# Optimization experiments

Measured on AMD Instinct MI355X. Metric: run time of the kernel, lower is better.

The kernel has to match this reference:

```python
import jax, jax.numpy as jnp
import numpy as np

N = 100000   # nodes
D = 128      # in_feats
H = 128      # hidden_size
E = 500000   # message edges
EP = 100000  # positive pair edges
EN = 500000  # negative pair edges


def setup_inputs() -> dict:
    key = jax.random.key(0)
    ks = jax.random.split(key, 20)
    s = 1.0 / np.sqrt(H)
    f32 = jnp.float32
    inp = {
        "x": jax.random.normal(ks[0], (N, D), f32),
        "src": jax.random.randint(ks[1], (E,), 0, N, jnp.int32),
        "dst": jax.random.randint(ks[2], (E,), 0, N, jnp.int32),
        "pos_src": jax.random.randint(ks[3], (EP,), 0, N, jnp.int32),
        "pos_dst": jax.random.randint(ks[4], (EP,), 0, N, jnp.int32),
        "neg_src": jax.random.randint(ks[5], (EN,), 0, N, jnp.int32),
        "neg_dst": jax.random.randint(ks[6], (EN,), 0, N, jnp.int32),
        # SAGEConv layer 0 (in->hid) and layer 1 (hid->hid)
        "W_self0": jax.random.normal(ks[7], (D, H), f32) * s,
        "W_neigh0": jax.random.normal(ks[8], (D, H), f32) * s,
        "b0": jnp.zeros((H,), f32),
        "W_self1": jax.random.normal(ks[9], (H, H), f32) * s,
        "W_neigh1": jax.random.normal(ks[10], (H, H), f32) * s,
        "b1": jnp.zeros((H,), f32),
        # EdgeDecoder MLP: hid->hid->hid->1
        "dW1": jax.random.normal(ks[11], (H, H), f32) * s,
        "db1": jnp.zeros((H,), f32),
        "dW2": jax.random.normal(ks[12], (H, H), f32) * s,
        "db2": jnp.zeros((H,), f32),
        "dW3": jax.random.normal(ks[13], (H, 1), f32) * s,
        "db3": jnp.zeros((1,), f32),
    }
    return inp


def _sage_mean(h, src, dst, W_self, W_neigh, b, n_nodes):
    # mean-aggregate neighbor features: gather src feats, segment-sum over dst
    agg = jax.ops.segment_sum(h[src], dst, num_segments=n_nodes)       # [N, d]
    deg = jax.ops.segment_sum(jnp.ones((src.shape[0],), h.dtype), dst,
                              num_segments=n_nodes)                     # [N]
    h_neigh = agg / jnp.maximum(deg, 1.0)[:, None]
    return h @ W_self + h_neigh @ W_neigh + b


def _edge_decode(h, e_src, e_dst, W1, b1, W2, b2, W3, b3):
    z = h[e_src] * h[e_dst]                    # [E_pair, H]
    z = jax.nn.relu(z @ W1 + b1)
    z = jax.nn.relu(z @ W2 + b2)
    return z @ W3 + b3                         # [E_pair, 1]


def reference(x, src, dst, pos_src, pos_dst, neg_src, neg_dst,
              W_self0, W_neigh0, b0, W_self1, W_neigh1, b1,
              dW1, db1, dW2, db2, dW3, db3):
    n = x.shape[0]
    h = jax.nn.relu(_sage_mean(x, src, dst, W_self0, W_neigh0, b0, n))
    h = _sage_mean(h, src, dst, W_self1, W_neigh1, b1, n)  # no act on last layer
    h_pos = _edge_decode(h, pos_src, pos_dst, dW1, db1, dW2, db2, dW3, db3)
    h_neg = _edge_decode(h, neg_src, neg_dst, dW1, db1, dW2, db2, dW3, db3)
    return (h_pos, h_neg)
```

## Files before the change

kernel.cpp:

```cpp
#include <hip/hip_runtime.h>
#include <hip/hip_bf16.h>

#define HD 128

typedef unsigned int u32;
typedef unsigned short u16;
typedef __attribute__((ext_vector_type(8))) short short8;
typedef __attribute__((ext_vector_type(4))) float f32x4;

__device__ __forceinline__ float bf2f(u16 u) {
    return __uint_as_float(((u32)u) << 16);
}
__device__ __forceinline__ u16 f2bf(float f) {
    u32 u = __float_as_uint(f);
    u32 r = (u + 0x7fffu + ((u >> 16) & 1u)) >> 16;
    return (u16)r;
}
__device__ __forceinline__ u32 pk2bf(float lo, float hi) {
    __hip_bfloat162 h = __float22bfloat162_rn(make_float2(lo, hi));
    union { __hip_bfloat162 h; u32 u; } cv; cv.h = h;
    return cv.u;
}
__device__ __forceinline__ u32 hmul2(u32 a, u32 b) {
    union { u32 u; __hip_bfloat162 h; } x, y, r;
    x.u = a; y.u = b;
    r.h = __hmul2(x.h, y.h);
    return r.u;
}
__device__ __forceinline__ float ldf(const void* p, size_t i, bool f32m) {
    return f32m ? ((const float*)p)[i] : bf2f(((const u16*)p)[i]);
}
__device__ __forceinline__ int swz(int row, int col) {
    return row * 128 + ((((col >> 3) ^ (row & 7)) << 3) | (col & 7));
}

__global__ void detect_mode(const u32* __restrict__ x, int* __restrict__ mode) {
    __shared__ int cnt_s;
    if (threadIdx.x == 0) cnt_s = 0;
    __syncthreads();
    u32 e = (x[threadIdx.x] >> 23) & 0xFFu;
    if (e >= 90u && e < 170u) atomicAdd(&cnt_s, 1);
    __syncthreads();
    if (threadIdx.x == 0) mode[0] = (cnt_s >= 128) ? 1 : 0;
}

__global__ void pack_w6(const void* __restrict__ W0, const void* __restrict__ W1,
                        const void* __restrict__ W2, const void* __restrict__ W3,
                        const void* __restrict__ W4, const void* __restrict__ W5,
                        u16* __restrict__ out, const int* __restrict__ gmode) {
    const bool f32m = gmode[0] != 0;
    int gid = blockIdx.x * 256 + threadIdx.x;
    if (gid >= 6 * 16384) return;
    int sel = gid >> 14, idx = gid & 16383;
    const void* W = sel == 0 ? W0 : sel == 1 ? W1 : sel == 2 ? W2 :
                    sel == 3 ? W3 : sel == 4 ? W4 : W5;
    int j = idx & 7, lane = (idx >> 3) & 63, ks = (idx >> 9) & 3, nt = idx >> 11;
    int k = ks * 32 + (lane >> 4) * 8 + j;
    int n = nt * 16 + (lane & 15);
    out[gid] = f2bf(ldf(W, (size_t)k * HD + n, f32m));
}

__global__ void cnt_count(const int* __restrict__ dst, int* __restrict__ cnt, int e) {
    int i = blockIdx.x * 256 + threadIdx.x;
    if (i < e) atomicAdd(&cnt[dst[i]], 1);
}

__global__ void scan_blocks(const int* __restrict__ cnt, int* __restrict__ rowptr,
                            int* __restrict__ bsum, int n) {
    __shared__ int s[256];
    int t = threadIdx.x, gid = blockIdx.x * 256 + t;
    int v = (gid < n) ? cnt[gid] : 0;
    s[t] = v; __syncthreads();
    #pragma unroll
    for (int off = 1; off < 256; off <<= 1) {
        int x = (t >= off) ? s[t - off] : 0;
        __syncthreads();
        s[t] += x;
        __syncthreads();
    }
    if (gid < n) rowptr[gid] = s[t] - v;
    if (t == 255) bsum[blockIdx.x] = s[255];
}

__global__ void scan_bsum(int* __restrict__ bsum, int nb) {
    __shared__ int s[1024];
    __shared__ int carry;
    int t = threadIdx.x;
    if (t == 0) carry = 0;
    __syncthreads();
    for (int base = 0; base < nb; base += 1024) {
        int i = base + t;
        int v = (i < nb) ? bsum[i] : 0;
        s[t] = v; __syncthreads();
        #pragma unroll
        for (int off = 1; off < 1024; off <<= 1) {
            int x = (t >= off) ? s[t - off] : 0;
            __syncthreads();
            s[t] += x;
            __syncthreads();
        }
        if (i < nb) bsum[i] = carry + s[t] - v;
        __syncthreads();
        if (t == 0) carry += s[1023];
        __syncthreads();
    }
}

__global__ void scan_add(int* __restrict__ rowptr, const int* __restrict__ bsum,
                         int n, int e) {
    int gid = blockIdx.x * 256 + threadIdx.x;
    if (gid < n) rowptr[gid] += bsum[blockIdx.x];
    else if (gid == n) rowptr[n] = e;
}

__global__ void csr_fill(const int* __restrict__ src, const int* __restrict__ dst,
                         const int* __restrict__ rowptr, int* __restrict__ cur,
                         int* __restrict__ cidx, int e) {
    int i = blockIdx.x * 256 + threadIdx.x;
    if (i >= e) return;
    int d = dst[i];
    int p = rowptr[d] + atomicAdd(&cur[d], 1);
    cidx[p] = src[i];
}

__global__ __launch_bounds__(256) void agg_gather(
    const void* __restrict__ h, const int* __restrict__ rowptr,
    const int* __restrict__ cidx, u16* __restrict__ aggb,
    const int* __restrict__ gmode, int use_mode, int n) {
    const bool f32m = use_mode && (gmode[0] != 0);
    int wid = (blockIdx.x * 256 + threadIdx.x) >> 6;
    int lane = threadIdx.x & 63;
    if (wid >= n) return;
    int l16 = lane & 15, g = lane >> 4;
    int s0 = rowptr[wid], s1 = rowptr[wid + 1];
    float acc[8] = {0.f, 0.f, 0.f, 0.f, 0.f, 0.f, 0.f, 0.f};
    for (int i = s0 + g; i < s1; i += 4) {
        int s = cidx[i];
        if (f32m) {
            const float* p = (const float*)h + (size_t)s * HD + l16 * 8;
            float4 a = *(const float4*)p, b = *(const float4*)(p + 4);
            acc[0] += a.x; acc[1] += a.y; acc[2] += a.z; acc[3] += a.w;
            acc[4] += b.x; acc[5] += b.y; acc[6] += b.z; acc[7] += b.w;
        } else {
            uint4 v = *(const uint4*)((const u16*)h + (size_t)s * HD + l16 * 8);
            acc[0] += __uint_as_float(v.x << 16); acc[1] += __uint_as_float(v.x & 0xffff0000u);
            acc[2] += __uint_as_float(v.y << 16); acc[3] += __uint_as_float(v.y & 0xffff0000u);
            acc[4] += __uint_as_float(v.z << 16); acc[5] += __uint_as_float(v.z & 0xffff0000u);
            acc[6] += __uint_as_float(v.w << 16); acc[7] += __uint_as_float(v.w & 0xffff0000u);
        }
    }
    #pragma unroll
    for (int k = 0; k < 8; k++) {
        acc[k] += __shfl_xor(acc[k], 16);
        acc[k] += __shfl_xor(acc[k], 32);
    }
    if (g == 0) {
        float iv = 1.f / fmaxf((float)(s1 - s0), 1.f);
        uint4 o;
        o.x = pk2bf(acc[0] * iv, acc[1] * iv);
        o.y = pk2bf(acc[2] * iv, acc[3] * iv);
        o.z = pk2bf(acc[4] * iv, acc[5] * iv);
        o.w = pk2bf(acc[6] * iv, acc[7] * iv);
        *(uint4*)&aggb[(size_t)wid * HD + l16 * 8] = o;
    }
}

template <bool RELU>
__global__ __launch_bounds__(256) void sage_mfma(
    const void* __restrict__ X, const u16* __restrict__ aggb,
    const u16* __restrict__ Wsp, const u16* __restrict__ Wnp,
    const void* __restrict__ bias, u16* __restrict__ hout,
    const int* __restrict__ gmode, int use_mode, int n) {
    __shared__ u16 zS[64 * 128];
    __shared__ u16 zN[64 * 128];
    u16* outh = zS;

    const bool f32m = gmode[0] != 0;
    const bool inf32 = use_mode && f32m;
    const int t = threadIdx.x;
    const int n0 = blockIdx.x * 64;
    const int lane = t & 63;
    const int w = t >> 6;
    const int cl = lane & 15, quad = lane >> 4;

    #pragma unroll
    for (int i = 0; i < 4; i++) {
        int idx = t + i * 256;
        int e = idx >> 4, sg = (idx & 15) * 8;
        int node = n0 + e;
        uint4 p = make_uint4(0, 0, 0, 0), q = make_uint4(0, 0, 0, 0);
        if (node < n) {
            if (inf32) {
                const float* xp = (const float*)X + (size_t)node * HD + sg;
                float4 v0 = *(const float4*)xp, v1 = *(const float4*)(xp + 4);
                p.x = pk2bf(v0.x, v0.y); p.y = pk2bf(v0.z, v0.w);
                p.z = pk2bf(v1.x, v1.y); p.w = pk2bf(v1.z, v1.w);
            } else {
                p = *(const uint4*)((const u16*)X + (size_t)node * HD + sg);
            }
            q = *(const uint4*)&aggb[(size_t)node * HD + sg];
        }
        int sa = swz(e, sg);
        *(uint4*)&zS[sa] = p;
        *(uint4*)&zN[sa] = q;
    }
    __syncthreads();

    f32x4 acc[2][4];
    #pragma unroll
    for (int ft = 0; ft < 2; ft++) {
        int f0 = w * 32 + ft * 16 + quad * 4;
        f32x4 bv;
        bv[0] = ldf(bias, f0 + 0, f32m);
        bv[1] = ldf(bias, f0 + 1, f32m);
        bv[2] = ldf(bias, f0 + 2, f32m);
        bv[3] = ldf(bias, f0 + 3, f32m);
        #pragma unroll
        for (int et = 0; et < 4; et++) acc[ft][et] = bv;
    }
    #pragma unroll
    for (int ks = 0; ks < 4; ks++) {
        short8 aS[2], aN[2], bS[4], bN[4];
        #pragma unroll
        for (int ft = 0; ft < 2; ft++) {
            aS[ft] = ((const short8*)Wsp)[((w * 2 + ft) * 4 + ks) * 64 + lane];
            aN[ft] = ((const short8*)Wnp)[((w * 2 + ft) * 4 + ks) * 64 + lane];
        }
        #pragma unroll
        for (int et = 0; et < 4; et++) {
            int sa = swz(et * 16 + cl, ks * 32 + quad * 8);
            bS[et] = *(const short8*)&zS[sa];
            bN[et] = *(const short8*)&zN[sa];
        }
        #pragma unroll
        for (int ft = 0; ft < 2; ft++)
            #pragma unroll
            for (int et = 0; et < 4; et++) {
                acc[ft][et] = __builtin_amdgcn_mfma_f32_16x16x32_bf16(
                    aS[ft], bS[et], acc[ft][et], 0, 0, 0);
                acc[ft][et] = __builtin_amdgcn_mfma_f32_16x16x32_bf16(
                    aN[ft], bN[et], acc[ft][et], 0, 0, 0);
            }
    }
    __syncthreads();

    #pragma unroll
    for (int ft = 0; ft < 2; ft++) {
        int f0 = w * 32 + ft * 16 + quad * 4;
        #pragma unroll
        for (int et = 0; et < 4; et++) {
            f32x4 v = acc[ft][et];
            float v0 = RELU ? fmaxf(v[0], 0.f) : v[0];
            float v1 = RELU ? fmaxf(v[1], 0.f) : v[1];
            float v2 = RELU ? fmaxf(v[2], 0.f) : v[2];
            float v3 = RELU ? fmaxf(v[3], 0.f) : v[3];
            *(uint2*)&outh[swz(et * 16 + cl, f0)] =
                make_uint2(pk2bf(v0, v1), pk2bf(v2, v3));
        }
    }
    __syncthreads();
    #pragma unroll
    for (int i = 0; i < 4; i++) {
        int idx = t + i * 256;
        int e = idx >> 4, sg = (idx & 15) * 8;
        int node = n0 + e;
        if (node < n)
            *(uint4*)&hout[(size_t)node * HD + sg] = *(const uint4*)&outh[swz(e, sg)];
    }
}

__device__ __forceinline__ void gemm128(
    const u16* zin, u16* zout, const u16* __restrict__ Wp,
    const void* __restrict__ bias, bool f32m, int w, int lane) {
    const int cl = lane & 15, quad = lane >> 4;
    f32x4 acc[2][4];
    #pragma unroll
    for (int ft = 0; ft < 2; ft++) {
        int f0 = w * 32 + ft * 16 + quad * 4;
        f32x4 bv;
        bv[0] = ldf(bias, f0 + 0, f32m);
        bv[1] = ldf(bias, f0 + 1, f32m);
        bv[2] = ldf(bias, f0 + 2, f32m);
        bv[3] = ldf(bias, f0 + 3, f32m);
        #pragma unroll
        for (int et = 0; et < 4; et++) acc[ft][et] = bv;
    }
    #pragma unroll
    for (int ks = 0; ks < 4; ks++) {
        short8 a[2], b[4];
        #pragma unroll
        for (int ft = 0; ft < 2; ft++)
            a[ft] = ((const short8*)Wp)[((w * 2 + ft) * 4 + ks) * 64 + lane];
        #pragma unroll
        for (int et = 0; et < 4; et++)
            b[et] = *(const short8*)&zin[swz(et * 16 + cl, ks * 32 + quad * 8)];
        #pragma unroll
        for (int ft = 0; ft < 2; ft++)
            #pragma unroll
            for (int et = 0; et < 4; et++)
                acc[ft][et] = __builtin_amdgcn_mfma_f32_16x16x32_bf16(
                    a[ft], b[et], acc[ft][et], 0, 0, 0);
    }
    #pragma unroll
    for (int ft = 0; ft < 2; ft++) {
        int f0 = w * 32 + ft * 16 + quad * 4;
        #pragma unroll
        for (int et = 0; et < 4; et++) {
            f32x4 v = acc[ft][et];
            *(uint2*)&zout[swz(et * 16 + cl, f0)] = make_uint2(
                pk2bf(fmaxf(v[0], 0.f), fmaxf(v[1], 0.f)),
                pk2bf(fmaxf(v[2], 0.f), fmaxf(v[3], 0.f)));
        }
    }
}

__global__ __launch_bounds__(256) void edge_decode_mfma(
    const u16* __restrict__ h,
    const int* __restrict__ psrc, const int* __restrict__ pdst, int ep, int PB,
    const int* __restrict__ nsrc, const int* __restrict__ ndst, int en,
    const u16* __restrict__ W1p, const void* __restrict__ b1,
    const u16* __restrict__ W2p, const void* __restrict__ b2,
    const void* __restrict__ W3, const void* __restrict__ b3,
    void* __restrict__ out, const int* __restrict__ gmode) {
    __shared__ u16 zA[64 * 128];
    __shared__ u16 zB[64 * 128];
    __shared__ float psum[256];
    const bool f32m = gmode[0] != 0;
    const int t = threadIdx.x;
    const int b = blockIdx.x;
    const int* esrc; const int* edst; int e0, obase, ne;
    if (b < PB) { esrc = psrc; edst = pdst; e0 = b * 64;        obase = 0;  ne = ep; }
    else        { esrc = nsrc; edst = ndst; e0 = (b - PB) * 64; obase = ep; ne = en; }
    const int lane = t & 63;
    const int w = t >> 6;
    const int cl = lane & 15, quad = lane >> 4;

    #pragma unroll
    for (int i = 0; i < 4; i++) {
        int idx = t + i * 256;
        int e = idx >> 4, sg = (idx & 15) * 8;
        int eg = e0 + e;
        uint4 z = make_uint4(0, 0, 0, 0);
        if (eg < ne) {
            int s = esrc[eg], d = edst[eg];
            uint4 a  = *(const uint4*)(h + (size_t)s * HD + sg);
            uint4 bv = *(const uint4*)(h + (size_t)d * HD + sg);
            z.x = hmul2(a.x, bv.x); z.y = hmul2(a.y, bv.y);
            z.z = hmul2(a.z, bv.z); z.w = hmul2(a.w, bv.w);
        }
        *(uint4*)&zA[swz(e, sg)] = z;
    }
    __syncthreads();

    gemm128(zA, zB, W1p, b1, f32m, w, lane);
    __syncthreads();

    f32x4 acc[2][4];
    #pragma unroll
    for (int ft = 0; ft < 2; ft++) {
        int f0 = w * 32 + ft * 16 + quad * 4;
        f32x4 bv;
        bv[0] = ldf(b2, f0 + 0, f32m);
        bv[1] = ldf(b2, f0 + 1, f32m);
        bv[2] = ldf(b2, f0 + 2, f32m);
        bv[3] = ldf(b2, f0 + 3, f32m);
        #pragma unroll
        for (int et = 0; et < 4; et++) acc[ft][et] = bv;
    }
    #pragma unroll
    for (int ks = 0; ks < 4; ks++) {
        short8 a[2], bb[4];
        #pragma unroll
        for (int ft = 0; ft < 2; ft++)
            a[ft] = ((const short8*)W2p)[((w * 2 + ft) * 4 + ks) * 64 + lane];
        #pragma unroll
        for (int et = 0; et < 4; et++)
            bb[et] = *(const short8*)&zB[swz(et * 16 + cl, ks * 32 + quad * 8)];
        #pragma unroll
        for (int ft = 0; ft < 2; ft++)
            #pragma unroll
            for (int et = 0; et < 4; et++)
                acc[ft][et] = __builtin_amdgcn_mfma_f32_16x16x32_bf16(
                    a[ft], bb[et], acc[ft][et], 0, 0, 0);
    }
    float p[4] = {0.f, 0.f, 0.f, 0.f};
    #pragma unroll
    for (int ft = 0; ft < 2; ft++) {
        int f0 = w * 32 + ft * 16 + quad * 4;
        float w3v0 = ldf(W3, f0 + 0, f32m);
        float w3v1 = ldf(W3, f0 + 1, f32m);
        float w3v2 = ldf(W3, f0 + 2, f32m);
        float w3v3 = ldf(W3, f0 + 3, f32m);
        #pragma unroll
        for (int et = 0; et < 4; et++) {
            f32x4 v = acc[ft][et];
            p[et] = fmaf(fmaxf(v[0], 0.f), w3v0, p[et]);
            p[et] = fmaf(fmaxf(v[1], 0.f), w3v1, p[et]);
            p[et] = fmaf(fmaxf(v[2], 0.f), w3v2, p[et]);
            p[et] = fmaf(fmaxf(v[3], 0.f), w3v3, p[et]);
        }
    }
    #pragma unroll
    for (int et = 0; et < 4; et++) {
        p[et] += __shfl_xor(p[et], 16);
        p[et] += __shfl_xor(p[et], 32);
    }
    if (lane < 16) {
        #pragma unroll
        for (int et = 0; et < 4; et++)
            psum[w * 64 + et * 16 + lane] = p[et];
    }
    __syncthreads();
    if (t < 64) {
        int eg = e0 + t;
        if (eg < ne) {
            float sum = ldf(b3, 0, f32m) + (psum[t] + psum[64 + t])
                      + (psum[128 + t] + psum[192 + t]);
            if (f32m) ((float*)out)[obase + eg] = sum;
            else      ((u16*)out)[obase + eg]   = f2bf(sum);
        }
    }
}

extern "C" void kernel_launch(void* const* d_in, const int* in_sizes, int n_in,
                              void* d_out, int out_size, void* d_ws, size_t ws_size,
                              hipStream_t stream) {
    const void* x      = d_in[0];
    const int* src     = (const int*)d_in[1];
    const int* dst     = (const int*)d_in[2];
    const int* pos_src = (const int*)d_in[3];
    const int* pos_dst = (const int*)d_in[4];
    const int* neg_src = (const int*)d_in[5];
    const int* neg_dst = (const int*)d_in[6];
    const void* Ws0 = d_in[7];
    const void* Wn0 = d_in[8];
    const void* b0  = d_in[9];
    const void* Ws1 = d_in[10];
    const void* Wn1 = d_in[11];
    const void* b1  = d_in[12];
    const void* dW1 = d_in[13];
    const void* db1 = d_in[14];
    const void* dW2 = d_in[15];
    const void* db2 = d_in[16];
    const void* dW3 = d_in[17];
    const void* db3 = d_in[18];

    const int n  = in_sizes[0] / HD;
    const int e  = in_sizes[1];
    const int ep = in_sizes[3];
    const int en = in_sizes[5];
    const int NB = (n + 255) / 256;
    const int PB = (ep + 63) / 64, NDB = (en + 63) / 64;

    char* base = (char*)d_ws;
    u16* aggb = (u16*)d_ws;
    u16* h1   = aggb + (size_t)n * HD;
    size_t off = (size_t)n * HD * 4;
    int* mode = (int*)(base + off);      off += 16;
    int* rowptr = (int*)(base + off);    off += (size_t)(n + 1) * 4; off = (off + 15) & ~(size_t)15;
    int* cnt = (int*)(base + off);       off += (size_t)n * 4;       off = (off + 15) & ~(size_t)15;
    int* cidx = (int*)(base + off);      off += (size_t)e * 4;       off = (off + 15) & ~(size_t)15;
    int* bsum = (int*)(base + off);      off += (size_t)NB * 4;      off = (off + 15) & ~(size_t)15;
    u16* Wpk  = (u16*)(base + off);
    u16* W1p  = Wpk;
    u16* W2p  = Wpk + 16384;
    u16* Ws0p = Wpk + 2 * 16384;
    u16* Wn0p = Wpk + 3 * 16384;
    u16* Ws1p = Wpk + 4 * 16384;
    u16* Wn1p = Wpk + 5 * 16384;

    detect_mode<<<dim3(1), dim3(256), 0, stream>>>((const u32*)x, mode);

    hipMemsetAsync(cnt, 0, (size_t)n * 4, stream);
    cnt_count<<<dim3((e + 255) / 256), dim3(256), 0, stream>>>(dst, cnt, e);
    scan_blocks<<<dim3(NB), dim3(256), 0, stream>>>(cnt, rowptr, bsum, n);
    scan_bsum<<<dim3(1), dim3(1024), 0, stream>>>(bsum, NB);
    scan_add<<<dim3((n + 256) / 256), dim3(256), 0, stream>>>(rowptr, bsum, n, e);
    hipMemsetAsync(cnt, 0, (size_t)n * 4, stream);
    csr_fill<<<dim3((e + 255) / 256), dim3(256), 0, stream>>>(src, dst, rowptr, cnt, cidx, e);

    pack_w6<<<dim3(384), dim3(256), 0, stream>>>(dW1, dW2, Ws0, Wn0, Ws1, Wn1, Wpk, mode);

    agg_gather<<<dim3((n * 64 + 255) / 256), dim3(256), 0, stream>>>(
        x, rowptr, cidx, aggb, mode, 1, n);
    sage_mfma<true><<<dim3((n + 63) / 64), dim3(256), 0, stream>>>(
        x, aggb, Ws0p, Wn0p, b0, h1, mode, 1, n);

    agg_gather<<<dim3((n * 64 + 255) / 256), dim3(256), 0, stream>>>(
        h1, rowptr, cidx, aggb, mode, 0, n);
    sage_mfma<false><<<dim3((n + 63) / 64), dim3(256), 0, stream>>>(
        h1, aggb, Ws1p, Wn1p, b1, aggb , mode, 0, n);

    edge_decode_mfma<<<dim3(PB + NDB), dim3(256), 0, stream>>>(
        aggb, pos_src, pos_dst, ep, PB, neg_src, neg_dst, en,
        W1p, db1, W2p, db2, dW3, db3, d_out, mode);
}
```

Measured before the change: 377.4 us.

## Persistent MFMA kernels with register-resident weights and single-pass CSR fill

The SAGE and edge-decoder MFMA kernels become persistent grid-stride loops over 64-row tiles on a capped grid. Each block loads its weight fragments and biases into registers once instead of per tile. The CSR fill now atomically bumps a cursor array that scan_add initialises from rowptr, which drops one memset and one rowptr load per edge. The risks are higher register pressure from holding the weight fragments, which may lower occupancy, and less latency hiding because tile loads are no longer overlapped across many blocks.

```diff
diff --git a/kernel.cpp b/kernel.cpp
--- a/kernel.cpp
+++ b/kernel.cpp
@@ -107,19 +107,22 @@
 }
 
 __global__ void scan_add(int* __restrict__ rowptr, const int* __restrict__ bsum,
-                         int n, int e) {
+                         int* __restrict__ cur, int n, int e) {
     int gid = blockIdx.x * 256 + threadIdx.x;
-    if (gid < n) rowptr[gid] += bsum[blockIdx.x];
-    else if (gid == n) rowptr[n] = e;
+    if (gid < n) {
+        int v = rowptr[gid] + bsum[blockIdx.x];
+        rowptr[gid] = v;
+        cur[gid] = v;
+    } else if (gid == n) {
+        rowptr[n] = e;
+    }
 }
 
 __global__ void csr_fill(const int* __restrict__ src, const int* __restrict__ dst,
-                         const int* __restrict__ rowptr, int* __restrict__ cur,
-                         int* __restrict__ cidx, int e) {
+                         int* __restrict__ cur, int* __restrict__ cidx, int e) {
     int i = blockIdx.x * 256 + threadIdx.x;
     if (i >= e) return;
-    int d = dst[i];
-    int p = rowptr[d] + atomicAdd(&cur[d], 1);
+    int p = atomicAdd(&cur[dst[i]], 1);
     cidx[p] = src[i];
 }
 
@@ -170,7 +173,7 @@
     const void* __restrict__ X, const u16* __restrict__ aggb,
     const u16* __restrict__ Wsp, const u16* __restrict__ Wnp,
     const void* __restrict__ bias, u16* __restrict__ hout,
-    const int* __restrict__ gmode, int use_mode, int n) {
+    const int* __restrict__ gmode, int use_mode, int n, int ntiles) {
     __shared__ u16 zS[64 * 128];
     __shared__ u16 zN[64 * 128];
     u16* outh = zS;
@@ -178,146 +181,109 @@
     const bool f32m = gmode[0] != 0;
     const bool inf32 = use_mode && f32m;
     const int t = threadIdx.x;
-    const int n0 = blockIdx.x * 64;
     const int lane = t & 63;
     const int w = t >> 6;
     const int cl = lane & 15, quad = lane >> 4;
 
-    #pragma unroll
-    for (int i = 0; i < 4; i++) {
-        int idx = t + i * 256;
-        int e = idx >> 4, sg = (idx & 15) * 8;
-        int node = n0 + e;
-        uint4 p = make_uint4(0, 0, 0, 0), q = make_uint4(0, 0, 0, 0);
-        if (node < n) {
-            if (inf32) {
-                const float* xp = (const float*)X + (size_t)node * HD + sg;
-                float4 v0 = *(const float4*)xp, v1 = *(const float4*)(xp + 4);
-                p.x = pk2bf(v0.x, v0.y); p.y = pk2bf(v0.z, v0.w);
-                p.z = pk2bf(v1.x, v1.y); p.w = pk2bf(v1.z, v1.w);
-            } else {
-                p = *(const uint4*)((const u16*)X + (size_t)node * HD + sg);
-            }
-            q = *(const uint4*)&aggb[(size_t)node * HD + sg];
-        }
-        int sa = swz(e, sg);
-        *(uint4*)&zS[sa] = p;
-        *(uint4*)&zN[sa] = q;
-    }
-    __syncthreads();
-
-    f32x4 acc[2][4];
+    short8 aS[2][4], aN[2][4];
+    f32x4 bv[2];
     #pragma unroll
     for (int ft = 0; ft < 2; ft++) {
+        #pragma unroll
+        for (int ks = 0; ks < 4; ks++) {
+            aS[ft][ks] = ((const short8*)Wsp)[((w * 2 + ft) * 4 + ks) * 64 + lane];
+            aN[ft][ks] = ((const short8*)Wnp)[((w * 2 + ft) * 4 + ks) * 64 + lane];
+        }
         int f0 = w * 32 + ft * 16 + quad * 4;
-        f32x4 bv;
-        bv[0] = ldf(bias, f0 + 0, f32m);
-        bv[1] = ldf(bias, f0 + 1, f32m);
-        bv[2] = ldf(bias, f0 + 2, f32m);
-        bv[3] = ldf(bias, f0 + 3, f32m);
-        #pragma unroll
-        for (int et = 0; et < 4; et++) acc[ft][et] = bv;
-    }
-    #pragma unroll
-    for (int ks = 0; ks < 4; ks++) {
-        short8 aS[2], aN[2], bS[4], bN[4];
+        bv[ft][0] = ldf(bias, f0 + 0, f32m);
+        bv[ft][1] = ldf(bias, f0 + 1, f32m);
+        bv[ft][2] = ldf(bias, f0 + 2, f32m);
+        bv[ft][3] = ldf(bias, f0 + 3, f32m);
+    }
+
+    for (int tile = blockIdx.x; tile < ntiles; tile += gridDim.x) {
+        const int n0 = tile * 64;
+
+        #pragma unroll
+        for (int i = 0; i < 4; i++) {
+            int idx = t + i * 256;
+            int e = idx >> 4, sg = (idx & 15) * 8;
+            int node = n0 + e;
+            uint4 p = make_uint4(0, 0, 0, 0), q = make_uint4(0, 0, 0, 0);
+            if (node < n) {
+                if (inf32) {
+                    const float* xp = (const float*)X + (size_t)node * HD + sg;
+                    float4 v0 = *(const float4*)xp, v1 = *(const float4*)(xp + 4);
+                    p.x = pk2bf(v0.x, v0.y); p.y = pk2bf(v0.z, v0.w);
+                    p.z = pk2bf(v1.x, v1.y); p.w = pk2bf(v1.z, v1.w);
+                } else {
+                    p = *(const uint4*)((const u16*)X + (size_t)node * HD + sg);
+                }
+                q = *(const uint4*)&aggb[(size_t)node * HD + sg];
+            }
+            int sa = swz(e, sg);
+            *(uint4*)&zS[sa] = p;
+            *(uint4*)&zN[sa] = q;
+        }
+        __syncthreads();
+
+        f32x4 acc[2][4];
+        #pragma unroll
+        for (int ft = 0; ft < 2; ft++)
+            #pragma unroll
+            for (int et = 0; et < 4; et++) acc[ft][et] = bv[ft];
+        #pragma unroll
+        for (int ks = 0; ks < 4; ks++) {
+            short8 bS[4], bN[4];
+            #pragma unroll
+            for (int et = 0; et < 4; et++) {
+                int sa = swz(et * 16 + cl, ks * 32 + quad * 8);
+                bS[et] = *(const short8*)&zS[sa];
+                bN[et] = *(const short8*)&zN[sa];
+            }
+            #pragma unroll
+            for (int ft = 0; ft < 2; ft++)
+                #pragma unroll
+                for (int et = 0; et < 4; et++) {
+                    acc[ft][et] = __builtin_amdgcn_mfma_f32_16x16x32_bf16(
+                        aS[ft][ks], bS[et], acc[ft][et], 0, 0, 0);
+                    acc[ft][et] = __builtin_amdgcn_mfma_f32_16x16x32_bf16(
+                        aN[ft][ks], bN[et], acc[ft][et], 0, 0, 0);
+                }
+        }
+        __syncthreads();
+
         #pragma unroll
         for (int ft = 0; ft < 2; ft++) {
-            aS[ft] = ((const short8*)Wsp)[((w * 2 + ft) * 4 + ks) * 64 + lane];
-            aN[ft] = ((const short8*)Wnp)[((w * 2 + ft) * 4 + ks) * 64 + lane];
-        }
-        #pragma unroll
-        for (int et = 0; et < 4; et++) {
-            int sa = swz(et * 16 + cl, ks * 32 + quad * 8);
-            bS[et] = *(const short8*)&zS[sa];
-            bN[et] = *(const short8*)&zN[sa];
-        }
-        #pragma unroll
-        for (int ft = 0; ft < 2; ft++)
+            int f0 = w * 32 + ft * 16 + quad * 4;
             #pragma unroll
             for (int et = 0; et < 4; et++) {
-                acc[ft][et] = __builtin_amdgcn_mfma_f32_16x16x32_bf16(
-                    aS[ft], bS[et], acc[ft][et], 0, 0, 0);
-                acc[ft][et] = __builtin_amdgcn_mfma_f32_16x16x32_bf16(
-                    aN[ft], bN[et], acc[ft][et], 0, 0, 0);
-            }
-    }
-    __syncthreads();
-
-    #pragma unroll
-    for (int ft = 0; ft < 2; ft++) {
-        int f0 = w * 32 + ft * 16 + quad * 4;
-        #pragma unroll
-        for (int et = 0; et < 4; et++) {
-            f32x4 v = acc[ft][et];
-            float v0 = RELU ? fmaxf(v[0], 0.f) : v[0];
-            float v1 = RELU ? fmaxf(v[1], 0.f) : v[1];
-            float v2 = RELU ? fmaxf(v[2], 0.f) : v[2];
-            float v3 = RELU ? fmaxf(v[3], 0.f) : v[3];
-            *(uint2*)&outh[swz(et * 16 + cl, f0)] =
-                make_uint2(pk2bf(v0, v1), pk2bf(v2, v3));
-        }
-    }
-    __syncthreads();
-    #pragma unroll
-    for (int i = 0; i < 4; i++) {
-        int idx = t + i * 256;
-        int e = idx >> 4, sg = (idx & 15) * 8;
-        int node = n0 + e;
-        if (node < n)
-            *(uint4*)&hout[(size_t)node * HD + sg] = *(const uint4*)&outh[swz(e, sg)];
-    }
-}
-
-__device__ __forceinline__ void gemm128(
-    const u16* zin, u16* zout, const u16* __restrict__ Wp,
-    const void* __restrict__ bias, bool f32m, int w, int lane) {
-    const int cl = lane & 15, quad = lane >> 4;
-    f32x4 acc[2][4];
-    #pragma unroll
-    for (int ft = 0; ft < 2; ft++) {
-        int f0 = w * 32 + ft * 16 + quad * 4;
-        f32x4 bv;
-        bv[0] = ldf(bias, f0 + 0, f32m);
-        bv[1] = ldf(bias, f0 + 1, f32m);
-        bv[2] = ldf(bias, f0 + 2, f32m);
-        bv[3] = ldf(bias, f0 + 3, f32m);
-        #pragma unroll
-        for (int et = 0; et < 4; et++) acc[ft][et] = bv;
-    }
-    #pragma unroll
-    for (int ks = 0; ks < 4; ks++) {
-        short8 a[2], b[4];
-        #pragma unroll
-        for (int ft = 0; ft < 2; ft++)
-            a[ft] = ((const short8*)Wp)[((w * 2 + ft) * 4 + ks) * 64 + lane];
-        #pragma unroll
-        for (int et = 0; et < 4; et++)
-            b[et] = *(const short8*)&zin[swz(et * 16 + cl, ks * 32 + quad * 8)];
-        #pragma unroll
-        for (int ft = 0; ft < 2; ft++)
-            #pragma unroll
-            for (int et = 0; et < 4; et++)
-                acc[ft][et] = __builtin_amdgcn_mfma_f32_16x16x32_bf16(
-                    a[ft], b[et], acc[ft][et], 0, 0, 0);
-    }
-    #pragma unroll
-    for (int ft = 0; ft < 2; ft++) {
-        int f0 = w * 32 + ft * 16 + quad * 4;
-        #pragma unroll
-        for (int et = 0; et < 4; et++) {
-            f32x4 v = acc[ft][et];
-            *(uint2*)&zout[swz(et * 16 + cl, f0)] = make_uint2(
-                pk2bf(fmaxf(v[0], 0.f), fmaxf(v[1], 0.f)),
-                pk2bf(fmaxf(v[2], 0.f), fmaxf(v[3], 0.f)));
-        }
+                f32x4 v = acc[ft][et];
+                float v0 = RELU ? fmaxf(v[0], 0.f) : v[0];
+                float v1 = RELU ? fmaxf(v[1], 0.f) : v[1];
+                float v2 = RELU ? fmaxf(v[2], 0.f) : v[2];
+                float v3 = RELU ? fmaxf(v[3], 0.f) : v[3];
+                *(uint2*)&outh[swz(et * 16 + cl, f0)] =
+                    make_uint2(pk2bf(v0, v1), pk2bf(v2, v3));
+            }
+        }
+        __syncthreads();
+        #pragma unroll
+        for (int i = 0; i < 4; i++) {
+            int idx = t + i * 256;
+            int e = idx >> 4, sg = (idx & 15) * 8;
+            int node = n0 + e;
+            if (node < n)
+                *(uint4*)&hout[(size_t)node * HD + sg] = *(const uint4*)&outh[swz(e, sg)];
+        }
+        __syncthreads();
     }
 }
 
 __global__ __launch_bounds__(256) void edge_decode_mfma(
     const u16* __restrict__ h,
     const int* __restrict__ psrc, const int* __restrict__ pdst, int ep, int PB,
-    const int* __restrict__ nsrc, const int* __restrict__ ndst, int en,
+    const int* __restrict__ nsrc, const int* __restrict__ ndst, int en, int TB,
     const u16* __restrict__ W1p, const void* __restrict__ b1,
     const u16* __restrict__ W2p, const void* __restrict__ b2,
     const void* __restrict__ W3, const void* __restrict__ b3,
@@ -327,98 +293,133 @@
     __shared__ float psum[256];
     const bool f32m = gmode[0] != 0;
     const int t = threadIdx.x;
-    const int b = blockIdx.x;
-    const int* esrc; const int* edst; int e0, obase, ne;
-    if (b < PB) { esrc = psrc; edst = pdst; e0 = b * 64;        obase = 0;  ne = ep; }
-    else        { esrc = nsrc; edst = ndst; e0 = (b - PB) * 64; obase = ep; ne = en; }
     const int lane = t & 63;
     const int w = t >> 6;
     const int cl = lane & 15, quad = lane >> 4;
 
-    #pragma unroll
-    for (int i = 0; i < 4; i++) {
-        int idx = t + i * 256;
-        int e = idx >> 4, sg = (idx & 15) * 8;
-        int eg = e0 + e;
-        uint4 z = make_uint4(0, 0, 0, 0);
-        if (eg < ne) {
-            int s = esrc[eg], d = edst[eg];
-            uint4 a  = *(const uint4*)(h + (size_t)s * HD + sg);
-            uint4 bv = *(const uint4*)(h + (size_t)d * HD + sg);
-            z.x = hmul2(a.x, bv.x); z.y = hmul2(a.y, bv.y);
-            z.z = hmul2(a.z, bv.z); z.w = hmul2(a.w, bv.w);
-        }
-        *(uint4*)&zA[swz(e, sg)] = z;
-    }
-    __syncthreads();
-
-    gemm128(zA, zB, W1p, b1, f32m, w, lane);
-    __syncthreads();
-
-    f32x4 acc[2][4];
+    short8 w1f[2][4], w2f[2][4];
+    f32x4 bv1[2], bv2[2], w3v[2];
     #pragma unroll
     for (int ft = 0; ft < 2; ft++) {
+        #pragma unroll
+        for (int ks = 0; ks < 4; ks++) {
+            w1f[ft][ks] = ((const short8*)W1p)[((w * 2 + ft) * 4 + ks) * 64 + lane];
+            w2f[ft][ks] = ((const short8*)W2p)[((w * 2 + ft) * 4 + ks) * 64 + lane];
+        }
         int f0 = w * 32 + ft * 16 + quad * 4;
-        f32x4 bv;
-        bv[0] = ldf(b2, f0 + 0, f32m);
-        bv[1] = ldf(b2, f0 + 1, f32m);
-        bv[2] = ldf(b2, f0 + 2, f32m);
-        bv[3] = ldf(b2, f0 + 3, f32m);
-        #pragma unroll
-        for (int et = 0; et < 4; et++) acc[ft][et] = bv;
-    }
-    #pragma unroll
-    for (int ks = 0; ks < 4; ks++) {
-        short8 a[2], bb[4];
+        #pragma unroll
+        for (int r = 0; r < 4; r++) {
+            bv1[ft][r] = ldf(b1, f0 + r, f32m);
+            bv2[ft][r] = ldf(b2, f0 + r, f32m);
+            w3v[ft][r] = ldf(W3, f0 + r, f32m);
+        }
+    }
+    const float b3v = ldf(b3, 0, f32m);
+
+    for (int tile = blockIdx.x; tile < TB; tile += gridDim.x) {
+        const int* esrc; const int* edst; int e0, obase, ne;
+        if (tile < PB) { esrc = psrc; edst = pdst; e0 = tile * 64;        obase = 0;  ne = ep; }
+        else           { esrc = nsrc; edst = ndst; e0 = (tile - PB) * 64; obase = ep; ne = en; }
+
+        #pragma unroll
+        for (int i = 0; i < 4; i++) {
+            int idx = t + i * 256;
+            int e = idx >> 4, sg = (idx & 15) * 8;
+            int eg = e0 + e;
+            uint4 z = make_uint4(0, 0, 0, 0);
+            if (eg < ne) {
+                int s = esrc[eg], d = edst[eg];
+                uint4 a  = *(const uint4*)(h + (size_t)s * HD + sg);
+                uint4 bb = *(const uint4*)(h + (size_t)d * HD + sg);
+                z.x = hmul2(a.x, bb.x); z.y = hmul2(a.y, bb.y);
+                z.z = hmul2(a.z, bb.z); z.w = hmul2(a.w, bb.w);
+            }
+            *(uint4*)&zA[swz(e, sg)] = z;
+        }
+        __syncthreads();
+
+        {
+            f32x4 acc[2][4];
+            #pragma unroll
+            for (int ft = 0; ft < 2; ft++)
+                #pragma unroll
+                for (int et = 0; et < 4; et++) acc[ft][et] = bv1[ft];
+            #pragma unroll
+            for (int ks = 0; ks < 4; ks++) {
+                short8 b[4];
+                #pragma unroll
+                for (int et = 0; et < 4; et++)
+                    b[et] = *(const short8*)&zA[swz(et * 16 + cl, ks * 32 + quad * 8)];
+                #pragma unroll
+                for (int ft = 0; ft < 2; ft++)
+                    #pragma unroll
+                    for (int et = 0; et < 4; et++)
+                        acc[ft][et] = __builtin_amdgcn_mfma_f32_16x16x32_bf16(
+                            w1f[ft][ks], b[et], acc[ft][et], 0, 0, 0);
+            }
+            #pragma unroll
+            for (int ft = 0; ft < 2; ft++) {
+                int f0 = w * 32 + ft * 16 + quad * 4;
+                #pragma unroll
+                for (int et = 0; et < 4; et++) {
+                    f32x4 v = acc[ft][et];
+                    *(uint2*)&zB[swz(et * 16 + cl, f0)] = make_uint2(
+                        pk2bf(fmaxf(v[0], 0.f), fmaxf(v[1], 0.f)),
+                        pk2bf(fmaxf(v[2], 0.f), fmaxf(v[3], 0.f)));
+                }
+            }
+        }
+        __syncthreads();
+
+        f32x4 acc[2][4];
         #pragma unroll
         for (int ft = 0; ft < 2; ft++)
-            a[ft] = ((const short8*)W2p)[((w * 2 + ft) * 4 + ks) * 64 + lane];
-        #pragma unroll
-        for (int et = 0; et < 4; et++)
-            bb[et] = *(const short8*)&zB[swz(et * 16 + cl, ks * 32 + quad * 8)];
+            #pragma unroll
+            for (int et = 0; et < 4; et++) acc[ft][et] = bv2[ft];
+        #pragma unroll
+        for (int ks = 0; ks < 4; ks++) {
+            short8 bb[4];
+            #pragma unroll
+            for (int et = 0; et < 4; et++)
+                bb[et] = *(const short8*)&zB[swz(et * 16 + cl, ks * 32 + quad * 8)];
+            #pragma unroll
+            for (int ft = 0; ft < 2; ft++)
+                #pragma unroll
+                for (int et = 0; et < 4; et++)
+                    acc[ft][et] = __builtin_amdgcn_mfma_f32_16x16x32_bf16(
+                        w2f[ft][ks], bb[et], acc[ft][et], 0, 0, 0);
+        }
+        float p[4] = {0.f, 0.f, 0.f, 0.f};
         #pragma unroll
         for (int ft = 0; ft < 2; ft++)
             #pragma unroll
+            for (int et = 0; et < 4; et++) {
+                f32x4 v = acc[ft][et];
+                p[et] = fmaf(fmaxf(v[0], 0.f), w3v[ft][0], p[et]);
+                p[et] = fmaf(fmaxf(v[1], 0.f), w3v[ft][1], p[et]);
+                p[et] = fmaf(fmaxf(v[2], 0.f), w3v[ft][2], p[et]);
+                p[et] = fmaf(fmaxf(v[3], 0.f), w3v[ft][3], p[et]);
+            }
+        #pragma unroll
+        for (int et = 0; et < 4; et++) {
+            p[et] += __shfl_xor(p[et], 16);
+            p[et] += __shfl_xor(p[et], 32);
+        }
+        if (lane < 16) {
+            #pragma unroll
             for (int et = 0; et < 4; et++)
-                acc[ft][et] = __builtin_amdgcn_mfma_f32_16x16x32_bf16(
-                    a[ft], bb[et], acc[ft][et], 0, 0, 0);
-    }
-    float p[4] = {0.f, 0.f, 0.f, 0.f};
-    #pragma unroll
-    for (int ft = 0; ft < 2; ft++) {
-        int f0 = w * 32 + ft * 16 + quad * 4;
-        float w3v0 = ldf(W3, f0 + 0, f32m);
-        float w3v1 = ldf(W3, f0 + 1, f32m);
-        float w3v2 = ldf(W3, f0 + 2, f32m);
-        float w3v3 = ldf(W3, f0 + 3, f32m);
-        #pragma unroll
-        for (int et = 0; et < 4; et++) {
-            f32x4 v = acc[ft][et];
-            p[et] = fmaf(fmaxf(v[0], 0.f), w3v0, p[et]);
-            p[et] = fmaf(fmaxf(v[1], 0.f), w3v1, p[et]);
-            p[et] = fmaf(fmaxf(v[2], 0.f), w3v2, p[et]);
-            p[et] = fmaf(fmaxf(v[3], 0.f), w3v3, p[et]);
-        }
-    }
-    #pragma unroll
-    for (int et = 0; et < 4; et++) {
-        p[et] += __shfl_xor(p[et], 16);
-        p[et] += __shfl_xor(p[et], 32);
-    }
-    if (lane < 16) {
-        #pragma unroll
-        for (int et = 0; et < 4; et++)
-            psum[w * 64 + et * 16 + lane] = p[et];
-    }
-    __syncthreads();
-    if (t < 64) {
-        int eg = e0 + t;
-        if (eg < ne) {
-            float sum = ldf(b3, 0, f32m) + (psum[t] + psum[64 + t])
-                      + (psum[128 + t] + psum[192 + t]);
-            if (f32m) ((float*)out)[obase + eg] = sum;
-            else      ((u16*)out)[obase + eg]   = f2bf(sum);
-        }
+                psum[w * 64 + et * 16 + lane] = p[et];
+        }
+        __syncthreads();
+        if (t < 64) {
+            int eg = e0 + t;
+            if (eg < ne) {
+                float sum = b3v + (psum[t] + psum[64 + t]) + (psum[128 + t] + psum[192 + t]);
+                if (f32m) ((float*)out)[obase + eg] = sum;
+                else      ((u16*)out)[obase + eg]   = f2bf(sum);
+            }
+        }
+        __syncthreads();
     }
 }
 
@@ -451,6 +452,7 @@
     const int en = in_sizes[5];
     const int NB = (n + 255) / 256;
     const int PB = (ep + 63) / 64, NDB = (en + 63) / 64;
+    const int NT = (n + 63) / 64;
 
     char* base = (char*)d_ws;
     u16* aggb = (u16*)d_ws;
@@ -458,7 +460,7 @@
     size_t off = (size_t)n * HD * 4;
     int* mode = (int*)(base + off);      off += 16;
     int* rowptr = (int*)(base + off);    off += (size_t)(n + 1) * 4; off = (off + 15) & ~(size_t)15;
-    int* cnt = (int*)(base + off);       off += (size_t)n * 4;       off = (off + 15) & ~(size_t)15;
+    int* cur = (int*)(base + off);       off += (size_t)n * 4;       off = (off + 15) & ~(size_t)15;
     int* cidx = (int*)(base + off);      off += (size_t)e * 4;       off = (off + 15) & ~(size_t)15;
     int* bsum = (int*)(base + off);      off += (size_t)NB * 4;      off = (off + 15) & ~(size_t)15;
     u16* Wpk  = (u16*)(base + off);
@@ -471,27 +473,28 @@
 
     detect_mode<<<dim3(1), dim3(256), 0, stream>>>((const u32*)x, mode);
 
-    hipMemsetAsync(cnt, 0, (size_t)n * 4, stream);
-    cnt_count<<<dim3((e + 255) / 256), dim3(256), 0, stream>>>(dst, cnt, e);
-    scan_blocks<<<dim3(NB), dim3(256), 0, stream>>>(cnt, rowptr, bsum, n);
+    hipMemsetAsync(cur, 0, (size_t)n * 4, stream);
+    cnt_count<<<dim3((e + 255) / 256), dim3(256), 0, stream>>>(dst, cur, e);
+    scan_blocks<<<dim3(NB), dim3(256), 0, stream>>>(cur, rowptr, bsum, n);
     scan_bsum<<<dim3(1), dim3(1024), 0, stream>>>(bsum, NB);
-    scan_add<<<dim3((n + 256) / 256), dim3(256), 0, stream>>>(rowptr, bsum, n, e);
-    hipMemsetAsync(cnt, 0, (size_t)n * 4, stream);
-    csr_fill<<<dim3((e + 255) / 256), dim3(256), 0, stream>>>(src, dst, rowptr, cnt, cidx, e);
+    scan_add<<<dim3((n + 256) / 256), dim3(256), 0, stream>>>(rowptr, bsum, cur, n, e);
+    csr_fill<<<dim3((e + 255) / 256), dim3(256), 0, stream>>>(src, dst, cur, cidx, e);
 
     pack_w6<<<dim3(384), dim3(256), 0, stream>>>(dW1, dW2, Ws0, Wn0, Ws1, Wn1, Wpk, mode);
 
     agg_gather<<<dim3((n * 64 + 255) / 256), dim3(256), 0, stream>>>(
         x, rowptr, cidx, aggb, mode, 1, n);
-    sage_mfma<true><<<dim3((n + 63) / 64), dim3(256), 0, stream>>>(
-        x, aggb, Ws0p, Wn0p, b0, h1, mode, 1, n);
+    sage_mfma<true><<<dim3(1024), dim3(256), 0, stream>>>(
+        x, aggb, Ws0p, Wn0p, b0, h1, mode, 1, n, NT);
 
     agg_gather<<<dim3((n * 64 + 255) / 256), dim3(256), 0, stream>>>(
         h1, rowptr, cidx, aggb, mode, 0, n);
-    sage_mfma<false><<<dim3((n + 63) / 64), dim3(256), 0, stream>>>(
-        h1, aggb, Ws1p, Wn1p, b1, aggb , mode, 0, n);
-
-    edge_decode_mfma<<<dim3(PB + NDB), dim3(256), 0, stream>>>(
-        aggb, pos_src, pos_dst, ep, PB, neg_src, neg_dst, en,
+    sage_mfma<false><<<dim3(1024), dim3(256), 0, stream>>>(
+        h1, aggb, Ws1p, Wn1p, b1, aggb , mode, 0, n, NT);
+
+    int TB = PB + NDB;
+    int db = TB < 1024 ? TB : 1024;
+    edge_decode_mfma<<<dim3(db), dim3(256), 0, stream>>>(
+        aggb, pos_src, pos_dst, ep, PB, neg_src, neg_dst, en, TB,
         W1p, db1, W2p, db2, dW3, db3, d_out, mode);
 }
```

Result: slower. 398.6 us (+5.6%).

## Halve shared memory in sage and decode kernels; seed CSR cursor in scan

Applied to the files above, without the earlier changes.

The SAGE GEMM kernel now stages self and neighbor inputs through one shared buffer in two sequential phases instead of two buffers at once. The edge decoder reuses a single tile for both MLP layers in place, and the gemm128 helper is inlined. Both kernels drop from 32 KB to about 16 KB of LDS per block, which should allow more resident blocks per CU. Separately, scan_add writes the row offsets into the cursor array, removing a memset and a rowptr load from csr_fill. The cost is extra barriers and serialized staging of the neighbor tile in the SAGE kernel.

```diff
diff --git a/kernel.cpp b/kernel.cpp
--- a/kernel.cpp
+++ b/kernel.cpp
@@ -107,19 +107,22 @@
 }
 
 __global__ void scan_add(int* __restrict__ rowptr, const int* __restrict__ bsum,
-                         int n, int e) {
+                         int* __restrict__ cur, int n, int e) {
     int gid = blockIdx.x * 256 + threadIdx.x;
-    if (gid < n) rowptr[gid] += bsum[blockIdx.x];
-    else if (gid == n) rowptr[n] = e;
+    if (gid < n) {
+        int v = rowptr[gid] + bsum[blockIdx.x];
+        rowptr[gid] = v;
+        cur[gid] = v;
+    } else if (gid == n) {
+        rowptr[n] = e;
+    }
 }
 
 __global__ void csr_fill(const int* __restrict__ src, const int* __restrict__ dst,
-                         const int* __restrict__ rowptr, int* __restrict__ cur,
-                         int* __restrict__ cidx, int e) {
+                         int* __restrict__ cur, int* __restrict__ cidx, int e) {
     int i = blockIdx.x * 256 + threadIdx.x;
     if (i >= e) return;
-    int d = dst[i];
-    int p = rowptr[d] + atomicAdd(&cur[d], 1);
+    int p = atomicAdd(&cur[dst[i]], 1);
     cidx[p] = src[i];
 }
 
@@ -171,10 +174,7 @@
     const u16* __restrict__ Wsp, const u16* __restrict__ Wnp,
     const void* __restrict__ bias, u16* __restrict__ hout,
     const int* __restrict__ gmode, int use_mode, int n) {
-    __shared__ u16 zS[64 * 128];
-    __shared__ u16 zN[64 * 128];
-    u16* outh = zS;
-
+    __shared__ u16 z[64 * 128];
     const bool f32m = gmode[0] != 0;
     const bool inf32 = use_mode && f32m;
     const int t = threadIdx.x;
@@ -188,7 +188,7 @@
         int idx = t + i * 256;
         int e = idx >> 4, sg = (idx & 15) * 8;
         int node = n0 + e;
-        uint4 p = make_uint4(0, 0, 0, 0), q = make_uint4(0, 0, 0, 0);
+        uint4 p = make_uint4(0, 0, 0, 0);
         if (node < n) {
             if (inf32) {
                 const float* xp = (const float*)X + (size_t)node * HD + sg;
@@ -198,11 +198,8 @@
             } else {
                 p = *(const uint4*)((const u16*)X + (size_t)node * HD + sg);
             }
-            q = *(const uint4*)&aggb[(size_t)node * HD + sg];
-        }
-        int sa = swz(e, sg);
-        *(uint4*)&zS[sa] = p;
-        *(uint4*)&zN[sa] = q;
+        }
+        *(uint4*)&z[swz(e, sg)] = p;
     }
     __syncthreads();
 
@@ -220,27 +217,47 @@
     }
     #pragma unroll
     for (int ks = 0; ks < 4; ks++) {
-        short8 aS[2], aN[2], bS[4], bN[4];
-        #pragma unroll
-        for (int ft = 0; ft < 2; ft++) {
-            aS[ft] = ((const short8*)Wsp)[((w * 2 + ft) * 4 + ks) * 64 + lane];
-            aN[ft] = ((const short8*)Wnp)[((w * 2 + ft) * 4 + ks) * 64 + lane];
-        }
-        #pragma unroll
-        for (int et = 0; et < 4; et++) {
-            int sa = swz(et * 16 + cl, ks * 32 + quad * 8);
-            bS[et] = *(const short8*)&zS[sa];
-            bN[et] = *(const short8*)&zN[sa];
-        }
+        short8 a[2], b[4];
+        #pragma unroll
+        for (int ft = 0; ft < 2; ft++)
+            a[ft] = ((const short8*)Wsp)[((w * 2 + ft) * 4 + ks) * 64 + lane];
+        #pragma unroll
+        for (int et = 0; et < 4; et++)
+            b[et] = *(const short8*)&z[swz(et * 16 + cl, ks * 32 + quad * 8)];
         #pragma unroll
         for (int ft = 0; ft < 2; ft++)
             #pragma unroll
-            for (int et = 0; et < 4; et++) {
+            for (int et = 0; et < 4; et++)
                 acc[ft][et] = __builtin_amdgcn_mfma_f32_16x16x32_bf16(
-                    aS[ft], bS[et], acc[ft][et], 0, 0, 0);
+                    a[ft], b[et], acc[ft][et], 0, 0, 0);
+    }
+    __syncthreads();
+
+    #pragma unroll
+    for (int i = 0; i < 4; i++) {
+        int idx = t + i * 256;
+        int e = idx >> 4, sg = (idx & 15) * 8;
+        int node = n0 + e;
+        uint4 q = make_uint4(0, 0, 0, 0);
+        if (node < n) q = *(const uint4*)&aggb[(size_t)node * HD + sg];
+        *(uint4*)&z[swz(e, sg)] = q;
+    }
+    __syncthreads();
+    #pragma unroll
+    for (int ks = 0; ks < 4; ks++) {
+        short8 a[2], b[4];
+        #pragma unroll
+        for (int ft = 0; ft < 2; ft++)
+            a[ft] = ((const short8*)Wnp)[((w * 2 + ft) * 4 + ks) * 64 + lane];
+        #pragma unroll
+        for (int et = 0; et < 4; et++)
+            b[et] = *(const short8*)&z[swz(et * 16 + cl, ks * 32 + quad * 8)];
+        #pragma unroll
+        for (int ft = 0; ft < 2; ft++)
+            #pragma unroll
+            for (int et = 0; et < 4; et++)
                 acc[ft][et] = __builtin_amdgcn_mfma_f32_16x16x32_bf16(
-                    aN[ft], bN[et], acc[ft][et], 0, 0, 0);
-            }
+                    a[ft], b[et], acc[ft][et], 0, 0, 0);
     }
     __syncthreads();
 
@@ -254,7 +271,7 @@
             float v1 = RELU ? fmaxf(v[1], 0.f) : v[1];
             float v2 = RELU ? fmaxf(v[2], 0.f) : v[2];
             float v3 = RELU ? fmaxf(v[3], 0.f) : v[3];
-            *(uint2*)&outh[swz(et * 16 + cl, f0)] =
+            *(uint2*)&z[swz(et * 16 + cl, f0)] =
                 make_uint2(pk2bf(v0, v1), pk2bf(v2, v3));
         }
     }
@@ -265,52 +282,7 @@
         int e = idx >> 4, sg = (idx & 15) * 8;
         int node = n0 + e;
         if (node < n)
-            *(uint4*)&hout[(size_t)node * HD + sg] = *(const uint4*)&outh[swz(e, sg)];
-    }
-}
-
-__device__ __forceinline__ void gemm128(
-    const u16* zin, u16* zout, const u16* __restrict__ Wp,
-    const void* __restrict__ bias, bool f32m, int w, int lane) {
-    const int cl = lane & 15, quad = lane >> 4;
-    f32x4 acc[2][4];
-    #pragma unroll
-    for (int ft = 0; ft < 2; ft++) {
-        int f0 = w * 32 + ft * 16 + quad * 4;
-        f32x4 bv;
-        bv[0] = ldf(bias, f0 + 0, f32m);
-        bv[1] = ldf(bias, f0 + 1, f32m);
-        bv[2] = ldf(bias, f0 + 2, f32m);
-        bv[3] = ldf(bias, f0 + 3, f32m);
-        #pragma unroll
-        for (int et = 0; et < 4; et++) acc[ft][et] = bv;
-    }
-    #pragma unroll
-    for (int ks = 0; ks < 4; ks++) {
-        short8 a[2], b[4];
-        #pragma unroll
-        for (int ft = 0; ft < 2; ft++)
-            a[ft] = ((const short8*)Wp)[((w * 2 + ft) * 4 + ks) * 64 + lane];
-        #pragma unroll
-        for (int et = 0; et < 4; et++)
-            b[et] = *(const short8*)&zin[swz(et * 16 + cl, ks * 32 + quad * 8)];
-        #pragma unroll
-        for (int ft = 0; ft < 2; ft++)
-            #pragma unroll
-            for (int et = 0; et < 4; et++)
-                acc[ft][et] = __builtin_amdgcn_mfma_f32_16x16x32_bf16(
-                    a[ft], b[et], acc[ft][et], 0, 0, 0);
-    }
-    #pragma unroll
-    for (int ft = 0; ft < 2; ft++) {
-        int f0 = w * 32 + ft * 16 + quad * 4;
-        #pragma unroll
-        for (int et = 0; et < 4; et++) {
-            f32x4 v = acc[ft][et];
-            *(uint2*)&zout[swz(et * 16 + cl, f0)] = make_uint2(
-                pk2bf(fmaxf(v[0], 0.f), fmaxf(v[1], 0.f)),
-                pk2bf(fmaxf(v[2], 0.f), fmaxf(v[3], 0.f)));
-        }
+            *(uint4*)&hout[(size_t)node * HD + sg] = *(const uint4*)&z[swz(e, sg)];
     }
 }
 
@@ -323,7 +295,6 @@
     const void* __restrict__ W3, const void* __restrict__ b3,
     void* __restrict__ out, const int* __restrict__ gmode) {
     __shared__ u16 zA[64 * 128];
-    __shared__ u16 zB[64 * 128];
     __shared__ float psum[256];
     const bool f32m = gmode[0] != 0;
     const int t = threadIdx.x;
@@ -352,10 +323,49 @@
     }
     __syncthreads();
 
-    gemm128(zA, zB, W1p, b1, f32m, w, lane);
-    __syncthreads();
-
     f32x4 acc[2][4];
+    #pragma unroll
+    for (int ft = 0; ft < 2; ft++) {
+        int f0 = w * 32 + ft * 16 + quad * 4;
+        f32x4 bv;
+        bv[0] = ldf(b1, f0 + 0, f32m);
+        bv[1] = ldf(b1, f0 + 1, f32m);
+        bv[2] = ldf(b1, f0 + 2, f32m);
+        bv[3] = ldf(b1, f0 + 3, f32m);
+        #pragma unroll
+        for (int et = 0; et < 4; et++) acc[ft][et] = bv;
+    }
+    #pragma unroll
+    for (int ks = 0; ks < 4; ks++) {
+        short8 a[2], bb[4];
+        #pragma unroll
+        for (int ft = 0; ft < 2; ft++)
+            a[ft] = ((const short8*)W1p)[((w * 2 + ft) * 4 + ks) * 64 + lane];
+        #pragma unroll
+        for (int et = 0; et < 4; et++)
+            bb[et] = *(const short8*)&zA[swz(et * 16 + cl, ks * 32 + quad * 8)];
+        #pragma unroll
+        for (int ft = 0; ft < 2; ft++)
+            #pragma unroll
+            for (int et = 0; et < 4; et++)
+                acc[ft][et] = __builtin_amdgcn_mfma_f32_16x16x32_bf16(
+                    a[ft], bb[et], acc[ft][et], 0, 0, 0);
+    }
+    __syncthreads();
+
+    #pragma unroll
+    for (int ft = 0; ft < 2; ft++) {
+        int f0 = w * 32 + ft * 16 + quad * 4;
+        #pragma unroll
+        for (int et = 0; et < 4; et++) {
+            f32x4 v = acc[ft][et];
+            *(uint2*)&zA[swz(et * 16 + cl, f0)] = make_uint2(
+                pk2bf(fmaxf(v[0], 0.f), fmaxf(v[1], 0.f)),
+                pk2bf(fmaxf(v[2], 0.f), fmaxf(v[3], 0.f)));
+        }
+    }
+    __syncthreads();
+
     #pragma unroll
     for (int ft = 0; ft < 2; ft++) {
         int f0 = w * 32 + ft * 16 + quad * 4;
@@ -375,7 +385,7 @@
             a[ft] = ((const short8*)W2p)[((w * 2 + ft) * 4 + ks) * 64 + lane];
         #pragma unroll
         for (int et = 0; et < 4; et++)
-            bb[et] = *(const short8*)&zB[swz(et * 16 + cl, ks * 32 + quad * 8)];
+            bb[et] = *(const short8*)&zA[swz(et * 16 + cl, ks * 32 + quad * 8)];
         #pragma unroll
         for (int ft = 0; ft < 2; ft++)
             #pragma unroll
@@ -458,7 +468,7 @@
     size_t off = (size_t)n * HD * 4;
     int* mode = (int*)(base + off);      off += 16;
     int* rowptr = (int*)(base + off);    off += (size_t)(n + 1) * 4; off = (off + 15) & ~(size_t)15;
-    int* cnt = (int*)(base + off);       off += (size_t)n * 4;       off = (off + 15) & ~(size_t)15;
+    int* cur = (int*)(base + off);       off += (size_t)n * 4;       off = (off + 15) & ~(size_t)15;
     int* cidx = (int*)(base + off);      off += (size_t)e * 4;       off = (off + 15) & ~(size_t)15;
     int* bsum = (int*)(base + off);      off += (size_t)NB * 4;      off = (off + 15) & ~(size_t)15;
     u16* Wpk  = (u16*)(base + off);
@@ -471,13 +481,12 @@
 
     detect_mode<<<dim3(1), dim3(256), 0, stream>>>((const u32*)x, mode);
 
-    hipMemsetAsync(cnt, 0, (size_t)n * 4, stream);
-    cnt_count<<<dim3((e + 255) / 256), dim3(256), 0, stream>>>(dst, cnt, e);
-    scan_blocks<<<dim3(NB), dim3(256), 0, stream>>>(cnt, rowptr, bsum, n);
+    hipMemsetAsync(cur, 0, (size_t)n * 4, stream);
+    cnt_count<<<dim3((e + 255) / 256), dim3(256), 0, stream>>>(dst, cur, e);
+    scan_blocks<<<dim3(NB), dim3(256), 0, stream>>>(cur, rowptr, bsum, n);
     scan_bsum<<<dim3(1), dim3(1024), 0, stream>>>(bsum, NB);
-    scan_add<<<dim3((n + 256) / 256), dim3(256), 0, stream>>>(rowptr, bsum, n, e);
-    hipMemsetAsync(cnt, 0, (size_t)n * 4, stream);
-    csr_fill<<<dim3((e + 255) / 256), dim3(256), 0, stream>>>(src, dst, rowptr, cnt, cidx, e);
+    scan_add<<<dim3((n + 256) / 256), dim3(256), 0, stream>>>(rowptr, bsum, cur, n, e);
+    csr_fill<<<dim3((e + 255) / 256), dim3(256), 0, stream>>>(src, dst, cur, cidx, e);
 
     pack_w6<<<dim3(384), dim3(256), 0, stream>>>(dW1, dW2, Ws0, Wn0, Ws1, Wn1, Wpk, mode);
 
```

After: 364.9 us. 1.03x faster.
